# Kernel tuning notes

Measured on AMD Instinct MI355X. Metric: run time of the kernel, lower is better.

## Reference

```python
import jax, jax.numpy as jnp
import numpy as np

D_MODEL = 2048
NUM_HEADS = 32
NUM_KV_HEADS = 8
HEAD_DIM = D_MODEL // NUM_HEADS  # 64
KV_GROUPS = NUM_HEADS // NUM_KV_HEADS  # 4


def setup_inputs() -> dict:
    key = jax.random.key(0)
    k1, k2, k3, k4, k5 = jax.random.split(key, 5)
    scale = 0.02
    h_bsd = jax.random.normal(k1, (2, 2048, D_MODEL), dtype=jnp.float32)
    # nn.Linear weights stored as [out_features, in_features]
    w_q = jax.random.normal(k2, (NUM_HEADS * HEAD_DIM, D_MODEL), dtype=jnp.float32) * scale
    w_k = jax.random.normal(k3, (NUM_KV_HEADS * HEAD_DIM, D_MODEL), dtype=jnp.float32) * scale
    w_v = jax.random.normal(k4, (NUM_KV_HEADS * HEAD_DIM, D_MODEL), dtype=jnp.float32) * scale
    w_o = jax.random.normal(k5, (D_MODEL, NUM_HEADS * HEAD_DIM), dtype=jnp.float32) * scale
    return {"h_bsd": h_bsd, "w_q": w_q, "w_k": w_k, "w_v": w_v, "w_o": w_o}


def reference(h_bsd, w_q, w_k, w_v, w_o):
    b, s, _ = h_bsd.shape
    # projections (Linear without bias: x @ W.T)
    q = (h_bsd @ w_q.T).reshape(b, s, NUM_HEADS, HEAD_DIM).transpose(0, 2, 1, 3)      # [b, nq, s, h]
    k = (h_bsd @ w_k.T).reshape(b, s, NUM_KV_HEADS, HEAD_DIM).transpose(0, 2, 1, 3)   # [b, nkv, l, h]
    v = (h_bsd @ w_v.T).reshape(b, s, NUM_KV_HEADS, HEAD_DIM).transpose(0, 2, 1, 3)   # [b, nkv, l, h]
    # repeat_interleave over head dim to expand kv heads to query heads
    k = jnp.repeat(k, KV_GROUPS, axis=1)  # [b, nq, l, h]
    v = jnp.repeat(v, KV_GROUPS, axis=1)
    attn = jnp.einsum('bqsh,bqlh->bqsl', q, k) / jnp.sqrt(jnp.float32(HEAD_DIM))
    attn = jax.nn.softmax(attn, axis=-1)
    out = jnp.einsum('bqsl,bqlh->bqsh', attn, v)            # [b, nq, s, h]
    out = out.transpose(0, 2, 1, 3).reshape(b, s, D_MODEL)  # [b, s, d]
    return out @ w_o.T
```

## Files before the change

kernel.cpp:

```cpp
#include <hip/hip_runtime.h>
#include <stdint.h>

typedef unsigned short ushort_t;
typedef __attribute__((ext_vector_type(8))) short short8;
typedef __attribute__((ext_vector_type(4))) float floatx4;


__device__ __forceinline__ ushort_t f2bf(float f) {
  unsigned int u = __builtin_bit_cast(unsigned int, f);
  u += 0x7fffu + ((u >> 16) & 1u);
  return (ushort_t)(u >> 16);
}

__device__ __forceinline__ void gld16(const void* g, void* l) {
  __builtin_amdgcn_global_load_lds(
      (__attribute__((address_space(1))) void*)(void*)(g),
      (__attribute__((address_space(3))) void*)(l), 16, 0, 0);
}


__global__ void cast_bf16_kernel(const float* __restrict__ in,
                                 ushort_t* __restrict__ out, int n4, float scale) {
  int i = blockIdx.x * 256 + threadIdx.x;
  if (i < n4) {
    float4 v = ((const float4*)in)[i];
    ushort4 o;
    o.x = f2bf(v.x * scale); o.y = f2bf(v.y * scale);
    o.z = f2bf(v.z * scale); o.w = f2bf(v.w * scale);
    ((ushort4*)out)[i] = o;
  }
}


template <int OM>
__global__ __launch_bounds__(256)
void gemm_bt(const ushort_t* __restrict__ A, const ushort_t* __restrict__ B,
             void* __restrict__ Cp, int M, int N, int K) {
  __shared__ ushort_t As[128 * 32];
  __shared__ ushort_t Bs[128 * 32];
  const int tid  = threadIdx.x;
  const int wave = tid >> 6, lane = tid & 63;
  const int quad = lane >> 4, l16 = lane & 15;
  const int wm = (wave >> 1) * 64, wn = (wave & 1) * 64;
  const int bm = blockIdx.x * 128, bn = blockIdx.y * 128;
  const int srow = lane >> 2, scc = lane & 3;

  floatx4 acc[4][4] = {};

  for (int k0 = 0; k0 < K; k0 += 32) {
#pragma unroll
    for (int r = 0; r < 2; ++r) {
      int c   = wave * 2 + r;
      int row = c * 16 + srow;
      int g   = scc ^ ((row >> 1) & 3);
      gld16(A + (long)(bm + row) * K + k0 + g * 8, As + c * 512 + lane * 8);
      gld16(B + (long)(bn + row) * K + k0 + g * 8, Bs + c * 512 + lane * 8);
    }
    __syncthreads();

    short8 af[4], bf[4];
#pragma unroll
    for (int i = 0; i < 4; ++i) {
      int m = wm + i * 16 + l16;
      af[i] = *(const short8*)(As + m * 32 + ((quad ^ ((m >> 1) & 3)) * 8));
      int n = wn + i * 16 + l16;
      bf[i] = *(const short8*)(Bs + n * 32 + ((quad ^ ((n >> 1) & 3)) * 8));
    }
#pragma unroll
    for (int i = 0; i < 4; ++i)
#pragma unroll
      for (int j = 0; j < 4; ++j)
        acc[i][j] = __builtin_amdgcn_mfma_f32_16x16x32_bf16(af[i], bf[j], acc[i][j], 0, 0, 0);
    __syncthreads();
  }

#pragma unroll
  for (int i = 0; i < 4; ++i)
#pragma unroll
    for (int j = 0; j < 4; ++j)
#pragma unroll
      for (int r = 0; r < 4; ++r) {
        int row = bm + wm + i * 16 + quad * 4 + r;
        int col = bn + wn + j * 16 + l16;
        if (OM == 0) ((ushort_t*)Cp)[(long)row * N + col] = f2bf(acc[i][j][r]);
        else         ((float*)Cp)[(long)row * N + col]    = acc[i][j][r];
      }
}


__global__ __launch_bounds__(256)
void transpose_v(const ushort_t* __restrict__ QKV, ushort_t* __restrict__ Vtg) {
  __shared__ ushort_t t[64 * 72];
  const int tid = threadIdx.x;
  const int b = blockIdx.z, kvh = blockIdx.y, l0 = blockIdx.x * 64;
#pragma unroll
  for (int r = 0; r < 2; ++r) {
    int idx = tid + r * 256;
    int row = idx >> 3, sub = idx & 7;
    short8 v = *(const short8*)(QKV + (long)(b * 2048 + l0 + row) * 3072 + 2560 + kvh * 64 + sub * 8);
    *(short8*)(t + row * 72 + sub * 8) = v;
  }
  __syncthreads();
#pragma unroll
  for (int r = 0; r < 2; ++r) {
    int idx = tid + r * 256;
    int hd = idx >> 3, sub = idx & 7;
    short8 o;
#pragma unroll
    for (int e = 0; e < 8; ++e) o[e] = (short)t[(sub * 8 + e) * 72 + hd];
    *(short8*)(Vtg + (long)((b * 8 + kvh) * 64 + hd) * 2048 + l0 + sub * 8) = o;
  }
}


__global__ __launch_bounds__(256)
void attn_kernel(const ushort_t* __restrict__ QKV, const ushort_t* __restrict__ Vtg,
                 ushort_t* __restrict__ AO) {
  __shared__ ushort_t Ks[64 * 64];
  __shared__ ushort_t Vt[64 * 64];
  __shared__ ushort_t Pt[128 * 64];
  __shared__ float    sumb[128];

  const int tid  = threadIdx.x;
  const int wave = tid >> 6, lane = tid & 63;
  const int quad = lane >> 4, l16 = lane & 15;
  const int b = blockIdx.z, h = blockIdx.y;
  const int q0 = blockIdx.x * 128;
  const int kvh = h >> 2;
  const long tok0 = (long)b * 2048 + q0;

  short8 qf[2][2];
#pragma unroll
  for (int kb = 0; kb < 2; ++kb)
#pragma unroll
    for (int j = 0; j < 2; ++j)
      qf[kb][j] = *(const short8*)(QKV + (tok0 + wave * 32 + j * 16 + l16) * 3072
                                   + h * 64 + kb * 32 + quad * 8);

  floatx4 oacc[2][4] = {};
  float lsum[2] = {0.f, 0.f};

  const int lr = lane >> 3, sub = lane & 7;
  const int g = sub ^ lr;
  const ushort_t* Kbase = QKV + (long)b * 2048 * 3072 + 2048 + kvh * 64;
  const ushort_t* Vbase = Vtg + (long)(b * 8 + kvh) * 64 * 2048;

  for (int l0 = 0; l0 < 2048; l0 += 64) {
    __syncthreads();
#pragma unroll
    for (int r = 0; r < 2; ++r) {
      int c = wave * 2 + r;
      int row = c * 8 + lr;
      gld16(Kbase + (long)(l0 + row) * 3072 + g * 8, Ks + c * 512 + lane * 8);
      gld16(Vbase + (long)row * 2048 + l0 + g * 8, Vt + c * 512 + lane * 8);
    }
    __syncthreads();

    floatx4 s[4][2] = {};
#pragma unroll
    for (int kb = 0; kb < 2; ++kb) {
      short8 kf[4];
#pragma unroll
      for (int i = 0; i < 4; ++i)
        kf[i] = *(const short8*)(Ks + (i * 16 + l16) * 64 + (((kb * 4 + quad) ^ (l16 & 7)) * 8));
#pragma unroll
      for (int i = 0; i < 4; ++i)
#pragma unroll
        for (int j = 0; j < 2; ++j)
          s[i][j] = __builtin_amdgcn_mfma_f32_16x16x32_bf16(kf[i], qf[kb][j], s[i][j], 0, 0, 0);
    }

#pragma unroll
    for (int i = 0; i < 4; ++i)
#pragma unroll
      for (int j = 0; j < 2; ++j) {
        float p0 = __expf(s[i][j][0]), p1 = __expf(s[i][j][1]);
        float p2 = __expf(s[i][j][2]), p3 = __expf(s[i][j][3]);
        lsum[j] += (p0 + p1) + (p2 + p3);
        ushort4 pk;
        pk.x = f2bf(p0); pk.y = f2bf(p1); pk.z = f2bf(p2); pk.w = f2bf(p3);
        int q = wave * 32 + j * 16 + l16;
        int idx = q * 64 + (((i * 2 + (quad >> 1)) ^ (l16 & 7)) * 8) + (quad & 1) * 4;
        *(ushort4*)(Pt + idx) = pk;
      }

#pragma unroll
    for (int kb = 0; kb < 2; ++kb) {
      short8 pf[2], vf[4];
#pragma unroll
      for (int im = 0; im < 2; ++im)
        pf[im] = *(const short8*)(Pt + (wave * 32 + im * 16 + l16) * 64
                                  + (((kb * 4 + quad) ^ (l16 & 7)) * 8));
#pragma unroll
      for (int n = 0; n < 4; ++n)
        vf[n] = *(const short8*)(Vt + (n * 16 + l16) * 64
                                 + (((kb * 4 + quad) ^ (l16 & 7)) * 8));
#pragma unroll
      for (int im = 0; im < 2; ++im)
#pragma unroll
        for (int n = 0; n < 4; ++n)
          oacc[im][n] = __builtin_amdgcn_mfma_f32_16x16x32_bf16(pf[im], vf[n], oacc[im][n], 0, 0, 0);
    }
  }

#pragma unroll
  for (int j = 0; j < 2; ++j) {
    float sv = lsum[j];
    sv += __shfl_xor(sv, 16);
    sv += __shfl_xor(sv, 32);
    if (quad == 0) sumb[wave * 32 + j * 16 + l16] = sv;
  }
  __syncthreads();

  float inv[2][4];
#pragma unroll
  for (int im = 0; im < 2; ++im)
#pragma unroll
    for (int r = 0; r < 4; ++r)
      inv[im][r] = 1.0f / sumb[wave * 32 + im * 16 + quad * 4 + r];

#pragma unroll
  for (int im = 0; im < 2; ++im)
#pragma unroll
    for (int n = 0; n < 4; ++n)
#pragma unroll
      for (int r = 0; r < 4; ++r) {
        long t = tok0 + wave * 32 + im * 16 + quad * 4 + r;
        AO[t * 2048 + h * 64 + n * 16 + l16] = f2bf(oacc[im][n][r] * inv[im][r]);
      }
}


extern "C" void kernel_launch(void* const* d_in, const int* in_sizes, int n_in,
                              void* d_out, int out_size, void* d_ws, size_t ws_size,
                              hipStream_t stream) {
  const float* h  = (const float*)d_in[0];
  const float* wq = (const float*)d_in[1];
  const float* wk = (const float*)d_in[2];
  const float* wv = (const float*)d_in[3];
  const float* wo = (const float*)d_in[4];
  float* out = (float*)d_out;

  const int BS = 4096, D = 2048, KV = 512, NQKV = 3072;

  ushort_t* h_bf    = (ushort_t*)d_ws;
  ushort_t* wqkv_bf = h_bf + (long)BS * D;
  ushort_t* wo_bf   = wqkv_bf + (long)NQKV * D;
  ushort_t* QKV     = wo_bf + (long)D * D;
  ushort_t* Vtg     = QKV + (long)BS * NQKV;
  ushort_t* AO      = h_bf;

  cast_bf16_kernel<<<(BS * D / 4 + 255) / 256, 256, 0, stream>>>(h, h_bf, BS * D / 4, 1.0f);
  cast_bf16_kernel<<<(D * D / 4 + 255) / 256, 256, 0, stream>>>(wq, wqkv_bf, D * D / 4, 0.125f);
  cast_bf16_kernel<<<(KV * D / 4 + 255) / 256, 256, 0, stream>>>(wk, wqkv_bf + (long)D * D, KV * D / 4, 1.0f);
  cast_bf16_kernel<<<(KV * D / 4 + 255) / 256, 256, 0, stream>>>(wv, wqkv_bf + (long)(D + KV) * D, KV * D / 4, 1.0f);
  cast_bf16_kernel<<<(D * D / 4 + 255) / 256, 256, 0, stream>>>(wo, wo_bf, D * D / 4, 1.0f);

  gemm_bt<0><<<dim3(BS / 128, NQKV / 128), 256, 0, stream>>>(h_bf, wqkv_bf, QKV, BS, NQKV, D);

  transpose_v<<<dim3(32, 8, 2), 256, 0, stream>>>(QKV, Vtg);

  attn_kernel<<<dim3(2048 / 128, 32, 2), 256, 0, stream>>>(QKV, Vtg, AO);

  gemm_bt<1><<<dim3(BS / 128, D / 128), 256, 0, stream>>>(AO, wo_bf, out, BS, D, D);
}
```

Measured before the change: 353.0 us.

## Fuse casts, double-buffer K/V tiles, use exp2 with log2e-scaled Q

```diff
diff --git a/kernel.cpp b/kernel.cpp
--- a/kernel.cpp
+++ b/kernel.cpp
@@ -19,16 +19,23 @@
 }
 
 
-__global__ void cast_bf16_kernel(const float* __restrict__ in,
-                                 ushort_t* __restrict__ out, int n4, float scale) {
-  int i = blockIdx.x * 256 + threadIdx.x;
-  if (i < n4) {
-    float4 v = ((const float4*)in)[i];
-    ushort4 o;
-    o.x = f2bf(v.x * scale); o.y = f2bf(v.y * scale);
-    o.z = f2bf(v.z * scale); o.w = f2bf(v.w * scale);
-    ((ushort4*)out)[i] = o;
-  }
+__global__ __launch_bounds__(256)
+void cast_all_kernel(const float* __restrict__ h, const float* __restrict__ wq,
+                     const float* __restrict__ wk, const float* __restrict__ wv,
+                     const float* __restrict__ wo,
+                     ushort_t* __restrict__ h_bf, ushort_t* __restrict__ wqkv_bf,
+                     ushort_t* __restrict__ wo_bf, float qscale) {
+  long i = (long)blockIdx.x * 256 + threadIdx.x;
+  const float4* src; ushort4* dst; float sc = 1.0f;
+  if (i < 2097152L)       { src = (const float4*)h  + i;             dst = (ushort4*)h_bf + i; }
+  else if (i < 3145728L)  { src = (const float4*)wq + (i - 2097152); dst = (ushort4*)wqkv_bf + (i - 2097152); sc = qscale; }
+  else if (i < 3407872L)  { src = (const float4*)wk + (i - 3145728); dst = (ushort4*)wqkv_bf + (i - 3145728) + 1048576; }
+  else if (i < 3670016L)  { src = (const float4*)wv + (i - 3407872); dst = (ushort4*)wqkv_bf + (i - 3407872) + 1310720; }
+  else                    { src = (const float4*)wo + (i - 3670016); dst = (ushort4*)wo_bf + (i - 3670016); }
+  float4 v = *src; ushort4 o;
+  o.x = f2bf(v.x * sc); o.y = f2bf(v.y * sc);
+  o.z = f2bf(v.z * sc); o.w = f2bf(v.w * sc);
+  *dst = o;
 }
 
 
@@ -116,8 +123,8 @@
 __global__ __launch_bounds__(256)
 void attn_kernel(const ushort_t* __restrict__ QKV, const ushort_t* __restrict__ Vtg,
                  ushort_t* __restrict__ AO) {
-  __shared__ ushort_t Ks[64 * 64];
-  __shared__ ushort_t Vt[64 * 64];
+  __shared__ ushort_t Ks[2][64 * 64];
+  __shared__ ushort_t Vt[2][64 * 64];
   __shared__ ushort_t Pt[128 * 64];
   __shared__ float    sumb[128];
 
@@ -145,16 +152,23 @@
   const ushort_t* Kbase = QKV + (long)b * 2048 * 3072 + 2048 + kvh * 64;
   const ushort_t* Vbase = Vtg + (long)(b * 8 + kvh) * 64 * 2048;
 
-  for (int l0 = 0; l0 < 2048; l0 += 64) {
-    __syncthreads();
+  auto stage = [&](int bf_, int l0) {
 #pragma unroll
     for (int r = 0; r < 2; ++r) {
       int c = wave * 2 + r;
       int row = c * 8 + lr;
-      gld16(Kbase + (long)(l0 + row) * 3072 + g * 8, Ks + c * 512 + lane * 8);
-      gld16(Vbase + (long)row * 2048 + l0 + g * 8, Vt + c * 512 + lane * 8);
-    }
+      gld16(Kbase + (long)(l0 + row) * 3072 + g * 8, Ks[bf_] + c * 512 + lane * 8);
+      gld16(Vbase + (long)row * 2048 + l0 + g * 8, Vt[bf_] + c * 512 + lane * 8);
+    }
+  };
+
+  stage(0, 0);
+
+  for (int it = 0; it < 32; ++it) {
     __syncthreads();
+    if (it + 1 < 32) stage((it + 1) & 1, (it + 1) * 64);
+    const ushort_t* Kc = Ks[it & 1];
+    const ushort_t* Vc = Vt[it & 1];
 
     floatx4 s[4][2] = {};
 #pragma unroll
@@ -162,7 +176,7 @@
       short8 kf[4];
 #pragma unroll
       for (int i = 0; i < 4; ++i)
-        kf[i] = *(const short8*)(Ks + (i * 16 + l16) * 64 + (((kb * 4 + quad) ^ (l16 & 7)) * 8));
+        kf[i] = *(const short8*)(Kc + (i * 16 + l16) * 64 + (((kb * 4 + quad) ^ (l16 & 7)) * 8));
 #pragma unroll
       for (int i = 0; i < 4; ++i)
 #pragma unroll
@@ -174,14 +188,19 @@
     for (int i = 0; i < 4; ++i)
 #pragma unroll
       for (int j = 0; j < 2; ++j) {
-        float p0 = __expf(s[i][j][0]), p1 = __expf(s[i][j][1]);
-        float p2 = __expf(s[i][j][2]), p3 = __expf(s[i][j][3]);
+        float p0 = __builtin_amdgcn_exp2f(s[i][j][0]);
+        float p1 = __builtin_amdgcn_exp2f(s[i][j][1]);
+        float p2 = __builtin_amdgcn_exp2f(s[i][j][2]);
+        float p3 = __builtin_amdgcn_exp2f(s[i][j][3]);
         lsum[j] += (p0 + p1) + (p2 + p3);
-        ushort4 pk;
-        pk.x = f2bf(p0); pk.y = f2bf(p1); pk.z = f2bf(p2); pk.w = f2bf(p3);
+        uint2 w;
+        w.x = __builtin_amdgcn_perm(__builtin_bit_cast(unsigned int, p1),
+                                    __builtin_bit_cast(unsigned int, p0), 0x07060302u);
+        w.y = __builtin_amdgcn_perm(__builtin_bit_cast(unsigned int, p3),
+                                    __builtin_bit_cast(unsigned int, p2), 0x07060302u);
         int q = wave * 32 + j * 16 + l16;
         int idx = q * 64 + (((i * 2 + (quad >> 1)) ^ (l16 & 7)) * 8) + (quad & 1) * 4;
-        *(ushort4*)(Pt + idx) = pk;
+        *(uint2*)(Pt + idx) = w;
       }
 
 #pragma unroll
@@ -193,7 +212,7 @@
                                   + (((kb * 4 + quad) ^ (l16 & 7)) * 8));
 #pragma unroll
       for (int n = 0; n < 4; ++n)
-        vf[n] = *(const short8*)(Vt + (n * 16 + l16) * 64
+        vf[n] = *(const short8*)(Vc + (n * 16 + l16) * 64
                                  + (((kb * 4 + quad) ^ (l16 & 7)) * 8));
 #pragma unroll
       for (int im = 0; im < 2; ++im)
@@ -250,11 +269,10 @@
   ushort_t* Vtg     = QKV + (long)BS * NQKV;
   ushort_t* AO      = h_bf;
 
-  cast_bf16_kernel<<<(BS * D / 4 + 255) / 256, 256, 0, stream>>>(h, h_bf, BS * D / 4, 1.0f);
-  cast_bf16_kernel<<<(D * D / 4 + 255) / 256, 256, 0, stream>>>(wq, wqkv_bf, D * D / 4, 0.125f);
-  cast_bf16_kernel<<<(KV * D / 4 + 255) / 256, 256, 0, stream>>>(wk, wqkv_bf + (long)D * D, KV * D / 4, 1.0f);
-  cast_bf16_kernel<<<(KV * D / 4 + 255) / 256, 256, 0, stream>>>(wv, wqkv_bf + (long)(D + KV) * D, KV * D / 4, 1.0f);
-  cast_bf16_kernel<<<(D * D / 4 + 255) / 256, 256, 0, stream>>>(wo, wo_bf, D * D / 4, 1.0f);
+  const float qscale = 0.125f * 1.44269504088896f;
+
+  cast_all_kernel<<<4718592 / 256, 256, 0, stream>>>(h, wq, wk, wv, wo,
+                                                     h_bf, wqkv_bf, wo_bf, qscale);
 
   gemm_bt<0><<<dim3(BS / 128, NQKV / 128), 256, 0, stream>>>(h_bf, wqkv_bf, QKV, BS, NQKV, D);
 
```

Measured after the change: 332.5 us. -5.8%, faster.
